# Performance work log

Measured on AMD Instinct MI355X. Metric: run time of the kernel, lower is better.

## Reference

```python
import jax, jax.numpy as jnp
import numpy as np

N_HEAD = 16
WINDOW = 256
GLOBAL = 32


def _sparse_mask(T):
    # local window of +/- WINDOW//2 plus global rows/cols for first GLOBAL tokens
    i = jnp.arange(T)
    local = jnp.abs(i[:, None] - i[None, :]) <= (WINDOW // 2)
    glob = (i[:, None] < GLOBAL) | (i[None, :] < GLOBAL)
    return local | glob  # [T, T] bool


def setup_inputs() -> dict:
    key = jax.random.key(0)
    k1, k2, k3 = jax.random.split(key, 3)
    B, T, C = 1, 4096, 1024
    scale = 0.02
    return {
        "x": jax.random.normal(k1, (B, T, C), dtype=jnp.float32),
        "W_attn": jax.random.normal(k2, (C, 3 * C), dtype=jnp.float32) * scale,
        "b_attn": jnp.zeros((3 * C,), dtype=jnp.float32),
        "W_proj": jax.random.normal(k3, (C, C), dtype=jnp.float32) * scale,
        "b_proj": jnp.zeros((C,), dtype=jnp.float32),
    }


def reference(x, W_attn, b_attn, W_proj, b_proj):
    B, T, C = x.shape
    H = N_HEAD
    D = C // H

    qkv = x @ W_attn + b_attn  # [B, T, 3C]
    q, k, v = jnp.split(qkv, 3, axis=-1)
    # [B, H, T, D]
    q = q.reshape(B, T, H, D).transpose(0, 2, 1, 3)
    k = k.reshape(B, T, H, D).transpose(0, 2, 1, 3)
    v = v.reshape(B, T, H, D).transpose(0, 2, 1, 3)

    mask = _sparse_mask(T)  # [T, T]
    att = jnp.einsum("bhqd,bhkd->bhqk", q, k) * (1.0 / np.sqrt(D))
    neg = jnp.finfo(att.dtype).min
    att = jnp.where(mask, att, neg)
    att = jax.nn.softmax(att, axis=-1)
    y = jnp.einsum("bhqk,bhkd->bhqd", att, v)  # [B, H, T, D]
    y = y.transpose(0, 2, 1, 3).reshape(B, T, C)
    return y @ W_proj + b_proj
```

## Files before the change

kernel.cpp:

```cpp
#include <hip/hip_runtime.h>
#include <hip/hip_bf16.h>
#include <math.h>

#define T_SEQ 4096
#define C_DIM 1024
#define H_HEADS 16
#define D_HEAD 64
#define QKVW 3072
#define WIN_HALF 128
#define GLOBAL_TOK 32

typedef __attribute__((ext_vector_type(8))) short bf16x8;
typedef __attribute__((ext_vector_type(4))) float f32x4;

__device__ __forceinline__ float bf2f(unsigned short u) {
    union { unsigned int i; float f; } c; c.i = ((unsigned int)u) << 16; return c.f;
}
__device__ __forceinline__ unsigned short f2bf(float f) {
    union { float f; unsigned int i; } c; c.f = f;
    return (unsigned short)((c.i + 0x7fffu + ((c.i >> 16) & 1u)) >> 16);
}

__device__ __forceinline__ void gll16(const unsigned short* g, unsigned short* l) {
    __builtin_amdgcn_global_load_lds(
        (const __attribute__((address_space(1))) void*)g,
        (__attribute__((address_space(3))) void*)l, 16, 0, 0);
}

__global__ __launch_bounds__(256) void cvt_f32_bf16_kernel(
    const float* __restrict__ src, unsigned short* __restrict__ dst, int n4)
{
    int idx = blockIdx.x * 256 + threadIdx.x;
    if (idx < n4) {
        float4 v = ((const float4*)src)[idx];
        ushort4 o;
        o.x = f2bf(v.x); o.y = f2bf(v.y); o.z = f2bf(v.z); o.w = f2bf(v.w);
        ((ushort4*)dst)[idx] = o;
    }
}

__global__ __launch_bounds__(256) void cvt_transpose_kernel(
    const float* __restrict__ src, unsigned short* __restrict__ dst,
    int R, int Ncols)
{
    __shared__ unsigned short tile[32][36];
    const int r0 = blockIdx.y * 32, c0 = blockIdx.x * 32;
    const int t = threadIdx.x;
    const int rr = t >> 3, cq = (t & 7) * 4;
    float4 v = *(const float4*)(src + (size_t)(r0 + rr) * Ncols + c0 + cq);
    tile[rr][cq + 0] = f2bf(v.x); tile[rr][cq + 1] = f2bf(v.y);
    tile[rr][cq + 2] = f2bf(v.z); tile[rr][cq + 3] = f2bf(v.w);
    __syncthreads();
    const int cc = t >> 3, rq = (t & 7) * 4;
    ushort4 o;
    o.x = tile[rq + 0][cc]; o.y = tile[rq + 1][cc];
    o.z = tile[rq + 2][cc]; o.w = tile[rq + 3][cc];
    *(ushort4*)(dst + (size_t)(c0 + cc) * R + r0 + rq) = o;
}

__global__ __launch_bounds__(256) void transpose_v_kernel(
    const unsigned short* __restrict__ qkv, unsigned short* __restrict__ vT)
{
    __shared__ unsigned short tile[32][36];
    const int c0 = blockIdx.x * 32;
    const int t0 = blockIdx.y * 32;
    const int t = threadIdx.x;
    const int rr = t >> 3, cq = (t & 7) * 4;
    ushort4 v = *(const ushort4*)(qkv + (size_t)(t0 + rr) * QKVW + 2 * C_DIM + c0 + cq);
    tile[rr][cq + 0] = v.x; tile[rr][cq + 1] = v.y;
    tile[rr][cq + 2] = v.z; tile[rr][cq + 3] = v.w;
    __syncthreads();
    const int cc = t >> 3, rq = (t & 7) * 4;
    ushort4 o;
    o.x = tile[rq + 0][cc]; o.y = tile[rq + 1][cc];
    o.z = tile[rq + 2][cc]; o.w = tile[rq + 3][cc];
    *(ushort4*)(vT + (size_t)(c0 + cc) * T_SEQ + t0 + rq) = o;
}

template<int OUT_BF16>
__global__ __launch_bounds__(256) void gemm_nt_kernel(
    const unsigned short* __restrict__ A,
    const unsigned short* __restrict__ Bt,
    const float* __restrict__ bias,
    void* __restrict__ Cv, int M, int N, int K)
{
    __shared__ unsigned short As[128 * 32];
    __shared__ unsigned short Bs[128 * 32];
    const int tid = threadIdx.x;
    const int w = tid >> 6, lane = tid & 63;
    const int quad = lane >> 4, r16 = lane & 15;
    const int m0 = blockIdx.y * 128, n0 = blockIdx.x * 128;
    const int wm = (w & 1) * 64, wn = (w >> 1) * 64;

    f32x4 acc[4][4];
    #pragma unroll
    for (int i = 0; i < 4; ++i)
        #pragma unroll
        for (int j = 0; j < 4; ++j) acc[i][j] = (f32x4){0.f, 0.f, 0.f, 0.f};

    const unsigned short* Ab = A + (size_t)m0 * K;
    const unsigned short* Bb = Bt + (size_t)n0 * K;

    for (int k0 = 0; k0 < K; k0 += 32) {
        __syncthreads();
        #pragma unroll
        for (int i = 0; i < 2; ++i) {
            const int chunk = w * 128 + i * 64 + lane;
            const int row = chunk >> 2, kc = (chunk & 3) * 8;
            gll16(Ab + (size_t)row * K + k0 + kc, &As[(w * 2 + i) * 512]);
            gll16(Bb + (size_t)row * K + k0 + kc, &Bs[(w * 2 + i) * 512]);
        }
        asm volatile("s_waitcnt vmcnt(0)" ::: "memory");
        __builtin_amdgcn_sched_barrier(0);
        __syncthreads();

        bf16x8 af[4], bf_[4];
        #pragma unroll
        for (int t = 0; t < 4; ++t) {
            af[t]  = *(const bf16x8*)&As[(wm + t * 16 + r16) * 32 + quad * 8];
            bf_[t] = *(const bf16x8*)&Bs[(wn + t * 16 + r16) * 32 + quad * 8];
        }
        #pragma unroll
        for (int mt = 0; mt < 4; ++mt)
            #pragma unroll
            for (int nt = 0; nt < 4; ++nt)
                acc[mt][nt] = __builtin_amdgcn_mfma_f32_16x16x32_bf16(
                    af[mt], bf_[nt], acc[mt][nt], 0, 0, 0);
    }

    #pragma unroll
    for (int nt = 0; nt < 4; ++nt) {
        const int col = n0 + wn + nt * 16 + r16;
        const float bv = bias[col];
        #pragma unroll
        for (int mt = 0; mt < 4; ++mt)
            #pragma unroll
            for (int reg = 0; reg < 4; ++reg) {
                const int row = m0 + wm + mt * 16 + quad * 4 + reg;
                if (OUT_BF16)
                    ((unsigned short*)Cv)[(size_t)row * N + col] = f2bf(acc[mt][nt][reg] + bv);
                else
                    ((float*)Cv)[(size_t)row * N + col] = acc[mt][nt][reg] + bv;
            }
    }
}

#define PT_STRIDE 72
#define NSLOT 8
#define PROW 72
__global__ __launch_bounds__(256, 4) void sparse_attn_mfma(
    const unsigned short* __restrict__ qkv,
    const unsigned short* __restrict__ vT,
    unsigned short* __restrict__ y,
    float* __restrict__ part)
{
    __shared__ unsigned short Pt[4][16 * PT_STRIDE];
    const int tid = threadIdx.x;
    const int w = tid >> 6, lane = tid & 63;
    const int quad = lane >> 4, n = lane & 15;
    const int bid = blockIdx.x;

    int h, rowbase, split = -1, rt = 0;
    if (bid < 1024) {
        h = bid & 15;
        const int rtile = (bid >> 4) * 4 + w;
        if (rtile < 2) return;
        rowbase = rtile * 16;
    } else {
        const int idx = bid - 1024;
        h = idx & 15;
        const int u = (idx >> 4) * 4 + w;
        rt = u >> 3; split = u & 7;
        rowbase = rt * 16;
    }
    const bool dense = split >= 0;

    int wlo = 0, n_tiles;
    if (dense) n_tiles = 8;
    else {
        int t0 = (rowbase - WIN_HALF) & ~63; if (t0 < 64) t0 = 64;
        wlo = t0;
        int whi = rowbase + 16 + WIN_HALF; if (whi > T_SEQ) whi = T_SEQ;
        n_tiles = 1 + (whi - wlo + 63) / 64;
    }

    const unsigned short* qp = qkv + (size_t)(rowbase + n) * QKVW + h * 64 + quad * 8;
    bf16x8 q0 = *(const bf16x8*)qp;
    bf16x8 q1 = *(const bf16x8*)(qp + 32);

    const unsigned short* kb = qkv + C_DIM + h * 64;
    const unsigned short* vb = vT + (size_t)h * 64 * T_SEQ;
    unsigned short* myPt = Pt[w];

    f32x4 O[4];
    #pragma unroll
    for (int i = 0; i < 4; ++i) O[i] = (f32x4){0.f, 0.f, 0.f, 0.f};
    float m_run = -INFINITY, l_run = 0.f;
    const int row = rowbase + n;

    for (int it = 0; it < n_tiles; ++it) {
        const int c0 = dense ? (split * 512 + it * 64)
                             : (it == 0 ? 0 : wlo + (it - 1) * 64);

        const unsigned short* kr = kb + (size_t)(c0 + n) * QKVW + quad * 8;
        bf16x8 klo[4], khi[4];
        #pragma unroll
        for (int g = 0; g < 4; ++g) {
            klo[g] = *(const bf16x8*)(kr + (size_t)(g * 16) * QKVW);
            khi[g] = *(const bf16x8*)(kr + (size_t)(g * 16) * QKVW + 32);
        }
        const f32x4 Z = (f32x4){0.f, 0.f, 0.f, 0.f};
        f32x4 St[4];
        #pragma unroll
        for (int g = 0; g < 4; ++g) {
            St[g] = __builtin_amdgcn_mfma_f32_16x16x32_bf16(klo[g], q0, Z, 0, 0, 0);
            St[g] = __builtin_amdgcn_mfma_f32_16x16x32_bf16(khi[g], q1, St[g], 0, 0, 0);
        }
        const unsigned short* vr = vb + (size_t)n * T_SEQ + c0 + quad * 8;
        bf16x8 vlo[4], vhi[4];
        #pragma unroll
        for (int d = 0; d < 4; ++d) {
            vlo[d] = *(const bf16x8*)(vr + (size_t)(d * 16) * T_SEQ);
            vhi[d] = *(const bf16x8*)(vr + (size_t)(d * 16) * T_SEQ + 32);
        }

        float mm = -INFINITY;
        #pragma unroll
        for (int g = 0; g < 4; ++g)
            #pragma unroll
            for (int r = 0; r < 4; ++r) {
                float v = St[g][r] * 0.125f;
                if (!dense) {
                    const int col = c0 + g * 16 + quad * 4 + r;
                    int dd = row - col; dd = dd < 0 ? -dd : dd;
                    if (!(col < GLOBAL_TOK || dd <= WIN_HALF)) v = -INFINITY;
                }
                St[g][r] = v;
                mm = fmaxf(mm, v);
            }
        mm = fmaxf(mm, __shfl_xor(mm, 16));
        mm = fmaxf(mm, __shfl_xor(mm, 32));
        const float mn = fmaxf(m_run, mm);
        const float mnf = (mn == -INFINITY) ? 0.f : mn;
        const float al = __expf(m_run - mnf);
        float rs = 0.f;
        #pragma unroll
        for (int g = 0; g < 4; ++g) {
            float e0 = __expf(St[g][0] - mnf);
            float e1 = __expf(St[g][1] - mnf);
            float e2 = __expf(St[g][2] - mnf);
            float e3 = __expf(St[g][3] - mnf);
            rs += (e0 + e1) + (e2 + e3);
            const unsigned int p01 = f2bf(e0) | ((unsigned int)f2bf(e1) << 16);
            const unsigned int p23 = f2bf(e2) | ((unsigned int)f2bf(e3) << 16);
            *(unsigned int*)&myPt[n * PT_STRIDE + g * 16 + quad * 4] = p01;
            *(unsigned int*)&myPt[n * PT_STRIDE + g * 16 + quad * 4 + 2] = p23;
        }
        rs += __shfl_xor(rs, 16);
        rs += __shfl_xor(rs, 32);
        l_run = l_run * al + rs;
        m_run = mn;
        #pragma unroll
        for (int d = 0; d < 4; ++d)
            #pragma unroll
            for (int r = 0; r < 4; ++r) O[d][r] *= al;

        asm volatile("s_waitcnt lgkmcnt(0)" ::: "memory");
        __builtin_amdgcn_sched_barrier(0);
        #pragma unroll
        for (int kg = 0; kg < 2; ++kg) {
            bf16x8 pf = *(const bf16x8*)&myPt[n * PT_STRIDE + kg * 32 + quad * 8];
            #pragma unroll
            for (int d = 0; d < 4; ++d)
                O[d] = __builtin_amdgcn_mfma_f32_16x16x32_bf16(
                    kg ? vhi[d] : vlo[d], pf, O[d], 0, 0, 0);
        }
    }

    if (!dense) {
        const float invL = 1.f / l_run;
        #pragma unroll
        for (int dblk = 0; dblk < 4; ++dblk)
            #pragma unroll
            for (int r = 0; r < 4; ++r)
                y[(size_t)row * C_DIM + h * 64 + dblk * 16 + quad * 4 + r] =
                    f2bf(O[dblk][r] * invL);
    } else {
        float* pb = part + ((size_t)(h * 2 + rt) * NSLOT + split) * 16 * PROW;
        #pragma unroll
        for (int dblk = 0; dblk < 4; ++dblk)
            #pragma unroll
            for (int r = 0; r < 4; ++r)
                pb[n * PROW + dblk * 16 + quad * 4 + r] = O[dblk][r];
        if (quad == 0) {
            pb[n * PROW + 64] = m_run;
            pb[n * PROW + 65] = l_run;
        }
    }
}

__global__ __launch_bounds__(64) void attn_combine(
    const float* __restrict__ part, unsigned short* __restrict__ y)
{
    const int d = threadIdx.x;
    const int h = blockIdx.x >> 1, rt = blockIdx.x & 1;
    const float* base = part + (size_t)(h * 2 + rt) * NSLOT * 16 * PROW;
    for (int row = 0; row < 16; ++row) {
        float M = -INFINITY;
        for (int sl = 0; sl < NSLOT; ++sl)
            M = fmaxf(M, base[(size_t)sl * 16 * PROW + row * PROW + 64]);
        float L = 0.f, Od = 0.f;
        for (int sl = 0; sl < NSLOT; ++sl) {
            const float* p = base + (size_t)sl * 16 * PROW + row * PROW;
            const float s = __expf(p[64] - M);
            L += p[65] * s;
            Od += p[d] * s;
        }
        y[(size_t)(rt * 16 + row) * C_DIM + h * 64 + d] = f2bf(Od / L);
    }
}

extern "C" void kernel_launch(void* const* d_in, const int* in_sizes, int n_in,
                              void* d_out, int out_size, void* d_ws, size_t ws_size,
                              hipStream_t stream) {
    const float* x  = (const float*)d_in[0];
    const float* Wa = (const float*)d_in[1];
    const float* ba = (const float*)d_in[2];
    const float* Wp = (const float*)d_in[3];
    const float* bp = (const float*)d_in[4];
    float* out = (float*)d_out;

    unsigned short* xb   = (unsigned short*)d_ws;
    unsigned short* Wabt = xb   + (size_t)T_SEQ * C_DIM;
    unsigned short* Wpbt = Wabt + (size_t)C_DIM * QKVW;
    unsigned short* qkv  = Wpbt + (size_t)C_DIM * C_DIM;
    unsigned short* yat  = qkv  + (size_t)T_SEQ * QKVW;
    unsigned short* vT = xb;
    float* part = (float*)Wabt;

    const int n_x = T_SEQ * C_DIM;
    cvt_f32_bf16_kernel<<<n_x / 4 / 256, 256, 0, stream>>>(x, xb, n_x / 4);
    cvt_transpose_kernel<<<dim3(QKVW / 32, C_DIM / 32), 256, 0, stream>>>(
        Wa, Wabt, C_DIM, QKVW);
    cvt_transpose_kernel<<<dim3(C_DIM / 32, C_DIM / 32), 256, 0, stream>>>(
        Wp, Wpbt, C_DIM, C_DIM);

    gemm_nt_kernel<1><<<dim3(QKVW / 128, T_SEQ / 128), 256, 0, stream>>>(
        xb, Wabt, ba, qkv, T_SEQ, QKVW, C_DIM);

    transpose_v_kernel<<<dim3(C_DIM / 32, T_SEQ / 32), 256, 0, stream>>>(qkv, vT);

    const int nBlocks = 1024 + 64;
    sparse_attn_mfma<<<nBlocks, 256, 0, stream>>>(qkv, vT, yat, part);
    attn_combine<<<H_HEADS * 2, 64, 0, stream>>>(part, yat);

    gemm_nt_kernel<0><<<dim3(C_DIM / 128, T_SEQ / 128), 256, 0, stream>>>(
        yat, Wpbt, bp, out, T_SEQ, C_DIM, C_DIM);
}
```

Before: 231.1 us.

## Double-buffer K/V register tiles and skip mask math on interior tiles

The attention loop now prefetches the next tile's K and V fragments into a second register buffer while the current tile's QK MFMAs and softmax run, ping-ponging between two buffers. Tiles that lie entirely inside the window skip the per-element mask computation, and the first global tile only masks its upper half statically. Launch bounds are relaxed from 4 to 2 blocks per CU so the extra registers fit, which lowers occupancy in exchange for more in-flight memory per wave.

```diff
diff --git a/kernel.cpp b/kernel.cpp
--- a/kernel.cpp
+++ b/kernel.cpp
@@ -148,7 +148,115 @@
 #define PT_STRIDE 72
 #define NSLOT 8
 #define PROW 72
-__global__ __launch_bounds__(256, 4) void sparse_attn_mfma(
+
+struct KVbuf { bf16x8 kl[4], kh[4], vl[4], vh[4]; };
+
+#define LOAD_KV(C0, B)                                                         \
+  {                                                                            \
+    const unsigned short* kr_ = kb + (size_t)((C0) + n) * QKVW + quad * 8;     \
+    _Pragma("unroll")                                                          \
+    for (int g = 0; g < 4; ++g) {                                              \
+      B.kl[g] = *(const bf16x8*)(kr_ + (size_t)(g * 16) * QKVW);               \
+      B.kh[g] = *(const bf16x8*)(kr_ + (size_t)(g * 16) * QKVW + 32);          \
+    }                                                                          \
+    const unsigned short* vr_ = vb + (size_t)n * T_SEQ + (C0) + quad * 8;      \
+    _Pragma("unroll")                                                          \
+    for (int d = 0; d < 4; ++d) {                                              \
+      B.vl[d] = *(const bf16x8*)(vr_ + (size_t)(d * 16) * T_SEQ);              \
+      B.vh[d] = *(const bf16x8*)(vr_ + (size_t)(d * 16) * T_SEQ + 32);         \
+    }                                                                          \
+  }
+
+#define PROC_TILE(ITV, CUR, NXT)                                               \
+  {                                                                            \
+    const int it_ = (ITV);                                                     \
+    const int c0 = dense ? (split * 512 + it_ * 64)                            \
+                         : (it_ == 0 ? 0 : wlo + (it_ - 1) * 64);              \
+    f32x4 St[4];                                                               \
+    _Pragma("unroll")                                                          \
+    for (int g = 0; g < 4; ++g) {                                              \
+      St[g] = __builtin_amdgcn_mfma_f32_16x16x32_bf16(CUR.kl[g], q0, Zf, 0, 0, 0); \
+      St[g] = __builtin_amdgcn_mfma_f32_16x16x32_bf16(CUR.kh[g], q1, St[g], 0, 0, 0); \
+    }                                                                          \
+    if (it_ + 1 < n_tiles) {                                                   \
+      const int c0n_ = dense ? (split * 512 + (it_ + 1) * 64)                  \
+                             : (it_ == 0 ? wlo : c0 + 64);                     \
+      LOAD_KV(c0n_, NXT);                                                      \
+    }                                                                          \
+    float mm = -INFINITY;                                                      \
+    const bool interior_ =                                                     \
+        dense || (it_ != 0 && c0 >= rowbase - 113 && c0 <= rowbase + 65);      \
+    if (interior_) {                                                           \
+      _Pragma("unroll")                                                        \
+      for (int g = 0; g < 4; ++g)                                              \
+        _Pragma("unroll")                                                      \
+        for (int r = 0; r < 4; ++r) {                                          \
+          const float v = St[g][r] * 0.125f;                                   \
+          St[g][r] = v; mm = fmaxf(mm, v);                                     \
+        }                                                                      \
+    } else if (it_ == 0 && rowbase >= 192) {                                   \
+      _Pragma("unroll")                                                        \
+      for (int g = 0; g < 2; ++g)                                              \
+        _Pragma("unroll")                                                      \
+        for (int r = 0; r < 4; ++r) {                                          \
+          const float v = St[g][r] * 0.125f;                                   \
+          St[g][r] = v; mm = fmaxf(mm, v);                                     \
+        }                                                                      \
+      _Pragma("unroll")                                                        \
+      for (int g = 2; g < 4; ++g)                                              \
+        _Pragma("unroll")                                                      \
+        for (int r = 0; r < 4; ++r) St[g][r] = -INFINITY;                      \
+    } else {                                                                   \
+      _Pragma("unroll")                                                        \
+      for (int g = 0; g < 4; ++g)                                              \
+        _Pragma("unroll")                                                      \
+        for (int r = 0; r < 4; ++r) {                                          \
+          float v = St[g][r] * 0.125f;                                         \
+          const int col = c0 + g * 16 + quad * 4 + r;                          \
+          int dd = row - col; dd = dd < 0 ? -dd : dd;                          \
+          if (!(col < GLOBAL_TOK || dd <= WIN_HALF)) v = -INFINITY;            \
+          St[g][r] = v; mm = fmaxf(mm, v);                                     \
+        }                                                                      \
+    }                                                                          \
+    mm = fmaxf(mm, __shfl_xor(mm, 16));                                        \
+    mm = fmaxf(mm, __shfl_xor(mm, 32));                                        \
+    const float mn = fmaxf(m_run, mm);                                         \
+    const float mnf = (mn == -INFINITY) ? 0.f : mn;                            \
+    const float al = __expf(m_run - mnf);                                      \
+    float rs = 0.f;                                                            \
+    _Pragma("unroll")                                                          \
+    for (int g = 0; g < 4; ++g) {                                              \
+      const float e0 = __expf(St[g][0] - mnf);                                 \
+      const float e1 = __expf(St[g][1] - mnf);                                 \
+      const float e2 = __expf(St[g][2] - mnf);                                 \
+      const float e3 = __expf(St[g][3] - mnf);                                 \
+      rs += (e0 + e1) + (e2 + e3);                                             \
+      const unsigned int p01 = f2bf(e0) | ((unsigned int)f2bf(e1) << 16);      \
+      const unsigned int p23 = f2bf(e2) | ((unsigned int)f2bf(e3) << 16);      \
+      *(unsigned int*)&myPt[n * PT_STRIDE + g * 16 + quad * 4] = p01;          \
+      *(unsigned int*)&myPt[n * PT_STRIDE + g * 16 + quad * 4 + 2] = p23;      \
+    }                                                                          \
+    rs += __shfl_xor(rs, 16);                                                  \
+    rs += __shfl_xor(rs, 32);                                                  \
+    l_run = l_run * al + rs;                                                   \
+    m_run = mn;                                                                \
+    _Pragma("unroll")                                                          \
+    for (int d = 0; d < 4; ++d)                                                \
+      _Pragma("unroll")                                                        \
+      for (int r = 0; r < 4; ++r) O[d][r] *= al;                               \
+    asm volatile("s_waitcnt lgkmcnt(0)" ::: "memory");                         \
+    __builtin_amdgcn_sched_barrier(0);                                         \
+    _Pragma("unroll")                                                          \
+    for (int kg = 0; kg < 2; ++kg) {                                           \
+      bf16x8 pf_ = *(const bf16x8*)&myPt[n * PT_STRIDE + kg * 32 + quad * 8];  \
+      _Pragma("unroll")                                                        \
+      for (int d = 0; d < 4; ++d)                                              \
+        O[d] = __builtin_amdgcn_mfma_f32_16x16x32_bf16(                        \
+            kg ? CUR.vh[d] : CUR.vl[d], pf_, O[d], 0, 0, 0);                   \
+    }                                                                          \
+  }
+
+__global__ __launch_bounds__(256, 2) void sparse_attn_mfma(
     const unsigned short* __restrict__ qkv,
     const unsigned short* __restrict__ vT,
     unsigned short* __restrict__ y,
@@ -197,84 +305,19 @@
     for (int i = 0; i < 4; ++i) O[i] = (f32x4){0.f, 0.f, 0.f, 0.f};
     float m_run = -INFINITY, l_run = 0.f;
     const int row = rowbase + n;
-
-    for (int it = 0; it < n_tiles; ++it) {
-        const int c0 = dense ? (split * 512 + it * 64)
-                             : (it == 0 ? 0 : wlo + (it - 1) * 64);
-
-        const unsigned short* kr = kb + (size_t)(c0 + n) * QKVW + quad * 8;
-        bf16x8 klo[4], khi[4];
-        #pragma unroll
-        for (int g = 0; g < 4; ++g) {
-            klo[g] = *(const bf16x8*)(kr + (size_t)(g * 16) * QKVW);
-            khi[g] = *(const bf16x8*)(kr + (size_t)(g * 16) * QKVW + 32);
-        }
-        const f32x4 Z = (f32x4){0.f, 0.f, 0.f, 0.f};
-        f32x4 St[4];
-        #pragma unroll
-        for (int g = 0; g < 4; ++g) {
-            St[g] = __builtin_amdgcn_mfma_f32_16x16x32_bf16(klo[g], q0, Z, 0, 0, 0);
-            St[g] = __builtin_amdgcn_mfma_f32_16x16x32_bf16(khi[g], q1, St[g], 0, 0, 0);
-        }
-        const unsigned short* vr = vb + (size_t)n * T_SEQ + c0 + quad * 8;
-        bf16x8 vlo[4], vhi[4];
-        #pragma unroll
-        for (int d = 0; d < 4; ++d) {
-            vlo[d] = *(const bf16x8*)(vr + (size_t)(d * 16) * T_SEQ);
-            vhi[d] = *(const bf16x8*)(vr + (size_t)(d * 16) * T_SEQ + 32);
-        }
-
-        float mm = -INFINITY;
-        #pragma unroll
-        for (int g = 0; g < 4; ++g)
-            #pragma unroll
-            for (int r = 0; r < 4; ++r) {
-                float v = St[g][r] * 0.125f;
-                if (!dense) {
-                    const int col = c0 + g * 16 + quad * 4 + r;
-                    int dd = row - col; dd = dd < 0 ? -dd : dd;
-                    if (!(col < GLOBAL_TOK || dd <= WIN_HALF)) v = -INFINITY;
-                }
-                St[g][r] = v;
-                mm = fmaxf(mm, v);
-            }
-        mm = fmaxf(mm, __shfl_xor(mm, 16));
-        mm = fmaxf(mm, __shfl_xor(mm, 32));
-        const float mn = fmaxf(m_run, mm);
-        const float mnf = (mn == -INFINITY) ? 0.f : mn;
-        const float al = __expf(m_run - mnf);
-        float rs = 0.f;
-        #pragma unroll
-        for (int g = 0; g < 4; ++g) {
-            float e0 = __expf(St[g][0] - mnf);
-            float e1 = __expf(St[g][1] - mnf);
-            float e2 = __expf(St[g][2] - mnf);
-            float e3 = __expf(St[g][3] - mnf);
-            rs += (e0 + e1) + (e2 + e3);
-            const unsigned int p01 = f2bf(e0) | ((unsigned int)f2bf(e1) << 16);
-            const unsigned int p23 = f2bf(e2) | ((unsigned int)f2bf(e3) << 16);
-            *(unsigned int*)&myPt[n * PT_STRIDE + g * 16 + quad * 4] = p01;
-            *(unsigned int*)&myPt[n * PT_STRIDE + g * 16 + quad * 4 + 2] = p23;
-        }
-        rs += __shfl_xor(rs, 16);
-        rs += __shfl_xor(rs, 32);
-        l_run = l_run * al + rs;
-        m_run = mn;
-        #pragma unroll
-        for (int d = 0; d < 4; ++d)
-            #pragma unroll
-            for (int r = 0; r < 4; ++r) O[d][r] *= al;
-
-        asm volatile("s_waitcnt lgkmcnt(0)" ::: "memory");
-        __builtin_amdgcn_sched_barrier(0);
-        #pragma unroll
-        for (int kg = 0; kg < 2; ++kg) {
-            bf16x8 pf = *(const bf16x8*)&myPt[n * PT_STRIDE + kg * 32 + quad * 8];
-            #pragma unroll
-            for (int d = 0; d < 4; ++d)
-                O[d] = __builtin_amdgcn_mfma_f32_16x16x32_bf16(
-                    kg ? vhi[d] : vlo[d], pf, O[d], 0, 0, 0);
-        }
+    const f32x4 Zf = (f32x4){0.f, 0.f, 0.f, 0.f};
+
+    KVbuf b0, b1;
+    {
+        const int c00 = dense ? (split * 512) : 0;
+        LOAD_KV(c00, b0);
+    }
+    int it = 0;
+    for (;;) {
+        PROC_TILE(it, b0, b1);
+        if (++it >= n_tiles) break;
+        PROC_TILE(it, b1, b0);
+        if (++it >= n_tiles) break;
     }
 
     if (!dense) {
```

Measured after the change: 224.0 us. 3.1% less time.
